# Kernel tuning notes

Hardware: AMD Instinct MI355X
Metric: run time of the kernel (lower is better)

Reference implementation:

```python
import jax, jax.numpy as jnp
import numpy as np

D_MODEL = 1024
EXPAND = 4
D_INNER = EXPAND * D_MODEL  # 4096
D_STATE = 16
D_CONV = 4
DT_RANK = (D_MODEL + 15) // 16  # 64
B_SZ, L_SEQ = 2, 2048
EPS = 1e-5


def _quantize(w):
    # round(clamp(w / mean|w|, -1, 1)) -> ternary weights
    s = w / (jnp.mean(jnp.abs(w)) + 1e-8)
    return jnp.round(jnp.clip(s, -1.0, 1.0))


def setup_inputs() -> dict:
    key = jax.random.key(0)
    ks = jax.random.split(key, 16)
    f32 = jnp.float32
    x = jax.random.normal(ks[0], (B_SZ, L_SEQ, D_MODEL), dtype=f32)
    # LayerNorms
    g1 = jnp.ones((D_MODEL,), f32); b1 = jnp.zeros((D_MODEL,), f32)
    g2 = jnp.ones((D_MODEL,), f32); b2 = jnp.zeros((D_MODEL,), f32)
    # SwiGLU MLP (ternary-quantized weights, as in __init__)
    w1 = _quantize(jax.random.normal(ks[1], (EXPAND * D_MODEL, D_MODEL), f32) * 0.02)
    bias1 = jnp.zeros((EXPAND * D_MODEL,), f32)
    w2 = _quantize(jax.random.normal(ks[2], (D_MODEL, EXPAND * D_MODEL), f32) * 0.02)
    bias2 = jnp.zeros((D_MODEL,), f32)
    # Mamba params
    in_proj_w = jax.random.normal(ks[3], (2 * D_INNER, D_MODEL), f32) * 0.02
    conv_w = jax.random.normal(ks[4], (D_INNER, D_CONV), f32) * 0.2
    conv_b = jnp.zeros((D_INNER,), f32)
    x_proj_w = jax.random.normal(ks[5], (DT_RANK + 2 * D_STATE, D_INNER), f32) * 0.02
    dt_proj_w = jax.random.normal(ks[6], (D_INNER, DT_RANK), f32) * (DT_RANK ** -0.5)
    dt_proj_b = jnp.log(jnp.expm1(jnp.clip(
        jnp.exp(jax.random.uniform(ks[7], (D_INNER,), f32) * (np.log(0.1) - np.log(1e-3)) + np.log(1e-3)),
        1e-4, None)))  # standard mamba dt bias init
    A_log = jnp.log(jnp.broadcast_to(jnp.arange(1, D_STATE + 1, dtype=f32), (D_INNER, D_STATE)))
    D = jnp.ones((D_INNER,), f32)
    out_proj_w = jax.random.normal(ks[8], (D_MODEL, D_INNER), f32) * 0.02
    return dict(x=x, g1=g1, b1=b1, g2=g2, b2=b2, w1=w1, bias1=bias1, w2=w2, bias2=bias2,
                in_proj_w=in_proj_w, conv_w=conv_w, conv_b=conv_b, x_proj_w=x_proj_w,
                dt_proj_w=dt_proj_w, dt_proj_b=dt_proj_b, A_log=A_log, D=D,
                out_proj_w=out_proj_w)


def _layernorm(x, g, b):
    mu = jnp.mean(x, -1, keepdims=True)
    var = jnp.mean(jnp.square(x - mu), -1, keepdims=True)
    return (x - mu) * jax.lax.rsqrt(var + EPS) * g + b


def _mamba(xn, in_proj_w, conv_w, conv_b, x_proj_w, dt_proj_w, dt_proj_b, A_log, D, out_proj_w):
    B, L, _ = xn.shape
    xz = jnp.einsum('bld,ed->ble', xn, in_proj_w)  # [B,L,2*d_inner]
    u, z = jnp.split(xz, 2, axis=-1)
    # causal depthwise conv1d, kernel size D_CONV
    up = jnp.pad(u, ((0, 0), (D_CONV - 1, 0), (0, 0)))
    conv = conv_b + sum(up[:, k:k + L, :] * conv_w[:, k] for k in range(D_CONV))
    u = jax.nn.silu(conv)  # [B,L,d_inner]
    x_dbl = jnp.einsum('bld,ed->ble', u, x_proj_w)
    dt_in, Bm, Cm = jnp.split(x_dbl, [DT_RANK, DT_RANK + D_STATE], axis=-1)
    dt = jax.nn.softplus(jnp.einsum('blr,dr->bld', dt_in, dt_proj_w) + dt_proj_b)
    A = -jnp.exp(A_log)  # [d_inner, d_state]

    def step(h, inp):
        dt_t, B_t, C_t, u_t = inp  # [B,d_inner],[B,d_state],[B,d_state],[B,d_inner]
        dA = jnp.exp(dt_t[..., None] * A)              # [B,d_inner,d_state]
        h = dA * h + (dt_t * u_t)[..., None] * B_t[:, None, :]
        y = jnp.einsum('bds,bs->bd', h, C_t)
        return h, y

    h0 = jnp.zeros((B, D_INNER, D_STATE), xn.dtype)
    xs = (dt.swapaxes(0, 1), Bm.swapaxes(0, 1), Cm.swapaxes(0, 1), u.swapaxes(0, 1))
    _, ys = jax.lax.scan(step, h0, xs)
    y = ys.swapaxes(0, 1) + u * D
    y = y * jax.nn.silu(z)
    return jnp.einsum('ble,de->bld', y, out_proj_w)


def reference(x, g1, b1, g2, b2, w1, bias1, w2, bias2, in_proj_w, conv_w, conv_b,
              x_proj_w, dt_proj_w, dt_proj_b, A_log, D, out_proj_w):
    h = _layernorm(x, g1, b1)
    h = jax.nn.silu(jnp.einsum('bld,ed->ble', h, w1) + bias1)
    x = x + jnp.einsum('ble,de->bld', h, w2) + bias2
    x = x + _mamba(_layernorm(x, g2, b2), in_proj_w, conv_w, conv_b, x_proj_w,
                   dt_proj_w, dt_proj_b, A_log, D, out_proj_w)
    return x
```

## Files before the change

kernel.cpp:

```cpp
#include <hip/hip_runtime.h>
#include <cstdint>
#include <cstddef>


namespace {
constexpr int D_MODEL = 1024;
constexpr int D_INNER = 4096;
constexpr int D_STATE = 16;
constexpr int DT_RANK = 64;
constexpr int B_SZ    = 2;
constexpr int L_SEQ   = 2048;
constexpr int M_ROWS  = B_SZ * L_SEQ;
constexpr int LC      = 64;
constexpr int NCHUNK  = L_SEQ / LC;
}

typedef __bf16 bf16x8_t __attribute__((ext_vector_type(8)));
typedef float  f32x4    __attribute__((ext_vector_type(4)));

__device__ __forceinline__ unsigned short f2bf(float f) {
  union { float f; unsigned int u; } v; v.f = f;
  unsigned int r = (v.u + 0x7fffu + ((v.u >> 16) & 1u)) >> 16;
  return (unsigned short)r;
}
__device__ __forceinline__ float bf2f(unsigned short s) {
  union { unsigned int u; float f; } v; v.u = ((unsigned int)s) << 16;
  return v.f;
}

__device__ __forceinline__ float softplus_fast(float v) {
  const float e = __builtin_amdgcn_exp2f(-fabsf(v) * 1.44269504088896f);
  return fmaxf(v, 0.f) + 0.693147180559945f * __builtin_amdgcn_logf(1.f + e);
}

__device__ __forceinline__ void gload16(const void* g, void* l) {
  __builtin_amdgcn_global_load_lds(
      (const __attribute__((address_space(1))) unsigned int*)g,
      (__attribute__((address_space(3))) unsigned int*)l, 16, 0, 0);
}

__global__ __launch_bounds__(256)
void cvt6(const float* __restrict__ s0, unsigned short* __restrict__ d0,
          const float* __restrict__ s1, unsigned short* __restrict__ d1,
          const float* __restrict__ s2, unsigned short* __restrict__ d2,
          const float* __restrict__ s3, unsigned short* __restrict__ d3,
          const float* __restrict__ s4, unsigned short* __restrict__ d4,
          const float* __restrict__ s5, unsigned short* __restrict__ d5) {
  int blk = blockIdx.x;
  const float* s; unsigned short* d;
  if (blk < 4096)                  { s = s0; d = d0; }
  else if ((blk -= 4096) < 4096)   { s = s1; d = d1; }
  else if ((blk -= 4096) < 8192)   { s = s2; d = d2; }
  else if ((blk -= 8192) < 384)    { s = s3; d = d3; }
  else if ((blk -= 384) < 256)     { s = s4; d = d4; }
  else { blk -= 256;                 s = s5; d = d5; }
  const int i = blk * 1024 + threadIdx.x * 4;
  float4 v = *(const float4*)(s + i);
  ushort4 o; o.x = f2bf(v.x); o.y = f2bf(v.y); o.z = f2bf(v.z); o.w = f2bf(v.w);
  *(ushort4*)(d + i) = o;
}

__global__ __launch_bounds__(256) void ln_bf16(const float* __restrict__ x,
                                               const float* __restrict__ g,
                                               const float* __restrict__ b,
                                               unsigned short* __restrict__ out) {
  const int row = blockIdx.x;
  const int tid = threadIdx.x;
  const float4 v = *(const float4*)(x + (size_t)row * D_MODEL + tid * 4);
  float s  = v.x + v.y + v.z + v.w;
  float s2 = v.x*v.x + v.y*v.y + v.z*v.z + v.w*v.w;
#pragma unroll
  for (int o = 32; o >= 1; o >>= 1) { s += __shfl_xor(s, o); s2 += __shfl_xor(s2, o); }
  __shared__ float red[8];
  if ((tid & 63) == 0) { red[(tid >> 6) * 2] = s; red[(tid >> 6) * 2 + 1] = s2; }
  __syncthreads();
  s  = red[0] + red[2] + red[4] + red[6];
  s2 = red[1] + red[3] + red[5] + red[7];
  const float mu  = s * (1.f / D_MODEL);
  const float var = s2 * (1.f / D_MODEL) - mu * mu;
  const float rstd = rsqrtf(var + 1e-5f);
  const float4 gv = *(const float4*)(g + tid * 4);
  const float4 bv = *(const float4*)(b + tid * 4);
  ushort4 o;
  o.x = f2bf((v.x - mu) * rstd * gv.x + bv.x);
  o.y = f2bf((v.y - mu) * rstd * gv.y + bv.y);
  o.z = f2bf((v.z - mu) * rstd * gv.z + bv.z);
  o.w = f2bf((v.w - mu) * rstd * gv.w + bv.w);
  *(ushort4*)(out + (size_t)row * D_MODEL + tid * 4) = o;
}

__global__ __launch_bounds__(256)
void combine_ln(const float* __restrict__ part, const float* __restrict__ bias,
                const float* __restrict__ res, const float* __restrict__ g,
                const float* __restrict__ b, float* __restrict__ x2out,
                unsigned short* __restrict__ xnout) {
  const int row = blockIdx.x;
  const int tid = threadIdx.x;
  const size_t i4 = (size_t)row * D_MODEL + tid * 4;
  constexpr size_t S = (size_t)M_ROWS * D_MODEL;
  const float4 p0 = *(const float4*)(part + i4);
  const float4 p1 = *(const float4*)(part + S + i4);
  const float4 p2 = *(const float4*)(part + 2 * S + i4);
  const float4 p3 = *(const float4*)(part + 3 * S + i4);
  const float4 bv = *(const float4*)(bias + tid * 4);
  const float4 rv = *(const float4*)(res + i4);
  float4 v;
  v.x = p0.x + p1.x + p2.x + p3.x + bv.x + rv.x;
  v.y = p0.y + p1.y + p2.y + p3.y + bv.y + rv.y;
  v.z = p0.z + p1.z + p2.z + p3.z + bv.z + rv.z;
  v.w = p0.w + p1.w + p2.w + p3.w + bv.w + rv.w;
  *(float4*)(x2out + i4) = v;
  float s  = v.x + v.y + v.z + v.w;
  float s2 = v.x*v.x + v.y*v.y + v.z*v.z + v.w*v.w;
#pragma unroll
  for (int o = 32; o >= 1; o >>= 1) { s += __shfl_xor(s, o); s2 += __shfl_xor(s2, o); }
  __shared__ float red[8];
  if ((tid & 63) == 0) { red[(tid >> 6) * 2] = s; red[(tid >> 6) * 2 + 1] = s2; }
  __syncthreads();
  s  = red[0] + red[2] + red[4] + red[6];
  s2 = red[1] + red[3] + red[5] + red[7];
  const float mu  = s * (1.f / D_MODEL);
  const float var = s2 * (1.f / D_MODEL) - mu * mu;
  const float rstd = rsqrtf(var + 1e-5f);
  const float4 gv = *(const float4*)(g + tid * 4);
  const float4 b2 = *(const float4*)(b + tid * 4);
  ushort4 o;
  o.x = f2bf((v.x - mu) * rstd * gv.x + b2.x);
  o.y = f2bf((v.y - mu) * rstd * gv.y + b2.y);
  o.z = f2bf((v.z - mu) * rstd * gv.z + b2.z);
  o.w = f2bf((v.w - mu) * rstd * gv.w + b2.w);
  *(ushort4*)(xnout + i4) = o;
}

template<int EPI>
__global__ __launch_bounds__(512, 1)
void gemm256(const unsigned short* __restrict__ A, const unsigned short* __restrict__ W,
             int M, int N, int K, int lda, int ldw,
             const float* __restrict__ bias, void* __restrict__ out0) {
  __shared__ unsigned short As[2][256 * 64];
  __shared__ unsigned short Bs[2][256 * 64];
  const int tid  = threadIdx.x;
  const int w    = tid >> 6;
  const int lane = tid & 63;
  const int wr = w >> 2;
  const int wc = w & 3;
  const int fr = lane & 15;
  const int fq = lane >> 4;

  const int gx = gridDim.x, gy = gridDim.y;
  const int nwg = gx * gy;
  const int id  = blockIdx.y * gx + blockIdx.x;
  const int wid = (id & 7) * (nwg >> 3) + (id >> 3);
  const int n0 = (wid / gy) * 256;
  const int m0 = (wid % gy) * 256;

  const int srow  = tid >> 3;
  const int skelem = ((tid & 7) ^ (srow & 7)) * 8;

  int aslot[2];
#pragma unroll
  for (int ks = 0; ks < 2; ++ks) aslot[ks] = ((ks * 4 + fq) ^ (fr & 7)) * 8;

  f32x4 acc[8][4];
#pragma unroll
  for (int m = 0; m < 8; ++m)
#pragma unroll
    for (int n = 0; n < 4; ++n) acc[m][n] = f32x4{0.f, 0.f, 0.f, 0.f};

  const int NT = K >> 6;

  auto STAGE_HALF = [&](int half, int tn, unsigned short* Ad, unsigned short* Bd) {
    const int k0 = tn * 64;
    if (half < 2) {
#pragma unroll
      for (int li = 0; li < 2; ++li) {
        const int l = half * 2 + li;
        gload16(A + (size_t)(m0 + l * 64 + srow) * lda + k0 + skelem,
                Ad + (l * 64 + w * 8) * 64);
      }
    } else {
#pragma unroll
      for (int li = 0; li < 2; ++li) {
        const int l = (half - 2) * 2 + li;
        gload16(W + (size_t)(n0 + l * 64 + srow) * ldw + k0 + skelem,
                Bd + (l * 64 + w * 8) * 64);
      }
    }
  };

#pragma unroll
  for (int h = 0; h < 4; ++h) STAGE_HALF(h, 0, &As[0][0], &Bs[0][0]);
  asm volatile("s_waitcnt vmcnt(0)" ::: "memory");
  __builtin_amdgcn_sched_barrier(0);
  __builtin_amdgcn_s_barrier();
  __builtin_amdgcn_sched_barrier(0);

  for (int t = 0; t < NT; ++t) {
    const int cur = t & 1;
    const unsigned short* Ab = &As[cur][0];
    const unsigned short* Bb = &Bs[cur][0];
    unsigned short* Adn = &As[cur ^ 1][0];
    unsigned short* Bdn = &Bs[cur ^ 1][0];
    const bool more = (t + 1 < NT);
#pragma unroll
    for (int p = 0; p < 4; ++p) {
      const int qm = p & 1, qn = p >> 1;
      bf16x8_t af[4][2], bf[2][2];
#pragma unroll
      for (int mfi = 0; mfi < 4; ++mfi)
#pragma unroll
        for (int ks = 0; ks < 2; ++ks)
          af[mfi][ks] = *(const bf16x8_t*)
              &Ab[(wr * 128 + (qm * 4 + mfi) * 16 + fr) * 64 + aslot[ks]];
#pragma unroll
      for (int nfi = 0; nfi < 2; ++nfi)
#pragma unroll
        for (int ks = 0; ks < 2; ++ks)
          bf[nfi][ks] = *(const bf16x8_t*)
              &Bb[(wc * 64 + (qn * 2 + nfi) * 16 + fr) * 64 + aslot[ks]];
      if (more) STAGE_HALF(p, t + 1, Adn, Bdn);
      asm volatile("s_waitcnt lgkmcnt(0)" ::: "memory");
      __builtin_amdgcn_sched_barrier(0);
      __builtin_amdgcn_s_barrier();
      __builtin_amdgcn_sched_barrier(0);
      __builtin_amdgcn_s_setprio(1);
#pragma unroll
      for (int mfi = 0; mfi < 4; ++mfi)
#pragma unroll
        for (int nfi = 0; nfi < 2; ++nfi)
#pragma unroll
          for (int ks = 0; ks < 2; ++ks)
            acc[qm * 4 + mfi][qn * 2 + nfi] = __builtin_amdgcn_mfma_f32_16x16x32_bf16(
                af[mfi][ks], bf[nfi][ks], acc[qm * 4 + mfi][qn * 2 + nfi], 0, 0, 0);
      __builtin_amdgcn_s_setprio(0);
      __builtin_amdgcn_sched_barrier(0);
    }
    asm volatile("s_waitcnt vmcnt(0)" ::: "memory");
    __builtin_amdgcn_sched_barrier(0);
    __builtin_amdgcn_s_barrier();
    __builtin_amdgcn_sched_barrier(0);
  }

#pragma unroll
  for (int mf = 0; mf < 8; ++mf)
#pragma unroll
    for (int nf = 0; nf < 4; ++nf)
#pragma unroll
      for (int j = 0; j < 4; ++j) {
        const int r = m0 + wr * 128 + mf * 16 + fq * 4 + j;
        const int c = n0 + wc * 64 + nf * 16 + fr;
        float v = acc[mf][nf][j];
        if constexpr (EPI == 0) {
          v += bias[c];
          v = v / (1.f + __expf(-v));
          ((unsigned short*)out0)[(size_t)r * N + c] = f2bf(v);
        } else {
          ((unsigned short*)out0)[(size_t)r * N + c] = f2bf(v);
        }
      }
}

template<int EPI>
__global__ __launch_bounds__(256)
void gemm_bt(const unsigned short* __restrict__ A, const unsigned short* __restrict__ W,
             int M, int N, int K, int lda, int ldw, int ldc,
             const float* __restrict__ bias, const float* __restrict__ res,
             void* __restrict__ out0) {
  if constexpr (EPI == 6 || EPI == 8) {
    const size_t koff = (size_t)blockIdx.z * K;
    A += koff; W += koff;
    if constexpr (EPI == 6)
      out0 = (void*)((float*)out0 + (size_t)blockIdx.z * M * ldc);
    else
      out0 = (void*)((unsigned short*)out0 + (size_t)blockIdx.z * M * ldc);
  }
  const int gx = gridDim.x, gy = gridDim.y;
  const int nwg = gx * gy;
  const int id  = blockIdx.y * gx + blockIdx.x;
  const int wid = (id & 7) * (nwg >> 3) + (id >> 3);
  const int n0 = (wid / gy) * 128;
  const int m0 = (wid % gy) * 128;

  __shared__ unsigned short As[2][128 * 32];
  __shared__ unsigned short Bs[2][128 * 32];
  const int tid  = threadIdx.x;
  const int w    = tid >> 6;
  const int lane = tid & 63;
  const int wm = (w >> 1) * 64;
  const int wn = (w & 1) * 64;
  const int lrow = lane >> 2;
  const int lkb  = (lane & 3) * 8;
  const int fr   = lane & 15;
  const int fq   = lane >> 4;

  f32x4 acc[4][4];
#pragma unroll
  for (int m = 0; m < 4; ++m)
#pragma unroll
    for (int n = 0; n < 4; ++n) acc[m][n] = f32x4{0.f, 0.f, 0.f, 0.f};

  const int ar0 = m0 + (w * 2 + 0) * 16 + lrow;
  const int ar1 = m0 + (w * 2 + 1) * 16 + lrow;
  int br0 = n0 + (w * 2 + 0) * 16 + lrow; if (br0 > N - 1) br0 = N - 1;
  int br1 = n0 + (w * 2 + 1) * 16 + lrow; if (br1 > N - 1) br1 = N - 1;

  const int nk = K >> 5;
  auto STAGE = [&](int buf, int kt) {
    const int k0 = kt * 32;
    gload16(A + (size_t)ar0 * lda + k0 + lkb, &As[buf][(w * 2 + 0) * 512]);
    gload16(A + (size_t)ar1 * lda + k0 + lkb, &As[buf][(w * 2 + 1) * 512]);
    gload16(W + (size_t)br0 * ldw + k0 + lkb, &Bs[buf][(w * 2 + 0) * 512]);
    gload16(W + (size_t)br1 * ldw + k0 + lkb, &Bs[buf][(w * 2 + 1) * 512]);
  };
  STAGE(0, 0);
  if (nk > 1) STAGE(1, 1);

  for (int kt = 0; kt < nk; ++kt) {
    const int cur = kt & 1;
    if (kt + 1 < nk) asm volatile("s_waitcnt vmcnt(4)" ::: "memory");
    else             asm volatile("s_waitcnt vmcnt(0)" ::: "memory");
    __builtin_amdgcn_sched_barrier(0);
    __builtin_amdgcn_s_barrier();
    __builtin_amdgcn_sched_barrier(0);
    bf16x8_t af[4], bf[4];
#pragma unroll
    for (int m = 0; m < 4; ++m) af[m] = *(const bf16x8_t*)&As[cur][(wm + m * 16 + fr) * 32 + fq * 8];
#pragma unroll
    for (int n = 0; n < 4; ++n) bf[n] = *(const bf16x8_t*)&Bs[cur][(wn + n * 16 + fr) * 32 + fq * 8];
    __builtin_amdgcn_s_setprio(1);
#pragma unroll
    for (int m = 0; m < 4; ++m)
#pragma unroll
      for (int n = 0; n < 4; ++n)
        acc[m][n] = __builtin_amdgcn_mfma_f32_16x16x32_bf16(af[m], bf[n], acc[m][n], 0, 0, 0);
    __builtin_amdgcn_s_setprio(0);
    __builtin_amdgcn_sched_barrier(0);
    asm volatile("s_waitcnt lgkmcnt(0)" ::: "memory");
    __builtin_amdgcn_s_barrier();
    __builtin_amdgcn_sched_barrier(0);
    if (kt + 2 < nk) STAGE(cur, kt + 2);
  }

#pragma unroll
  for (int m = 0; m < 4; ++m)
#pragma unroll
    for (int n = 0; n < 4; ++n)
#pragma unroll
      for (int j = 0; j < 4; ++j) {
        const int r = m0 + wm + m * 16 + fq * 4 + j;
        const int c = n0 + wn + n * 16 + fr;
        if (c >= N) continue;
        float v = acc[m][n][j];
        if constexpr (EPI == 4) {
          v = softplus_fast(v + bias[c]);
          ((unsigned short*)out0)[(size_t)r * ldc + c] = f2bf(v);
        } else if constexpr (EPI == 6) {
          ((float*)out0)[(size_t)r * ldc + c] = v;
        } else {
          ((unsigned short*)out0)[(size_t)r * ldc + c] = f2bf(v);
        }
      }
}

__global__ __launch_bounds__(256)
void splitk_combine_bf(const unsigned short* __restrict__ part,
                       const float* __restrict__ res, float* __restrict__ out) {
  const size_t i4 = ((size_t)blockIdx.x * 256 + threadIdx.x) * 4;
  constexpr size_t S = (size_t)M_ROWS * D_MODEL;
  float a0 = 0.f, a1 = 0.f, a2 = 0.f, a3 = 0.f;
#pragma unroll
  for (int z = 0; z < 4; ++z) {
    const ushort4 p = *(const ushort4*)(part + z * S + i4);
    a0 += bf2f(p.x); a1 += bf2f(p.y); a2 += bf2f(p.z); a3 += bf2f(p.w);
  }
  const float4 r = *(const float4*)(res + i4);
  *(float4*)(out + i4) = float4{a0 + r.x, a1 + r.y, a2 + r.z, a3 + r.w};
}

__global__ __launch_bounds__(256)
void conv_silu_k(const unsigned short* __restrict__ xz, const float* __restrict__ cw,
                 const float* __restrict__ cb, unsigned short* __restrict__ uc) {
  const size_t idx = (size_t)blockIdx.x * 256 + threadIdx.x;
  const int d   = (int)(idx & (D_INNER - 1));
  const int row = (int)(idx >> 12);
  const int l   = row & (L_SEQ - 1);
  const float4 w4 = *(const float4*)(cw + d * 4);
  const unsigned short* up = xz + (size_t)row * (2 * D_INNER) + d;
  float acc = cb[d];
  if (l >= 3) acc += bf2f(up[-(ptrdiff_t)3 * 2 * D_INNER]) * w4.x;
  if (l >= 2) acc += bf2f(up[-(ptrdiff_t)2 * 2 * D_INNER]) * w4.y;
  if (l >= 1) acc += bf2f(up[-(ptrdiff_t)1 * 2 * D_INNER]) * w4.z;
  acc += bf2f(up[0]) * w4.w;
  const float r = acc / (1.f + __expf(-acc));
  uc[(size_t)row * D_INNER + d] = f2bf(r);
}

__global__ __launch_bounds__(256)
void xproj_combine(const float* __restrict__ part, unsigned short* __restrict__ dtin,
                   float* __restrict__ Bm, float* __restrict__ Cm) {
  const int idx = blockIdx.x * 256 + threadIdx.x;
  const int r = idx / 96, c = idx - r * 96;
  constexpr size_t S = (size_t)M_ROWS * 96;
  const float v = part[idx] + part[idx + S] + part[idx + 2 * S] + part[idx + 3 * S];
  if (c < DT_RANK)            dtin[(size_t)r * DT_RANK + c] = f2bf(v);
  else if (c < DT_RANK + 16)  Bm[(size_t)r * 16 + (c - DT_RANK)] = v;
  else                        Cm[(size_t)r * 16 + (c - DT_RANK - 16)] = v;
}

__global__ __launch_bounds__(128)
void scan_part(const unsigned short* __restrict__ dt, const unsigned short* __restrict__ uc,
               const float* __restrict__ Bm, const float* __restrict__ A_log,
               float* __restrict__ Q, float* __restrict__ sumdt) {
  __shared__ float sB[LC][D_STATE];
  const int lt = threadIdx.x;
  const int d  = blockIdx.x * 128 + lt;
  const int c  = blockIdx.y;
  const int b  = blockIdx.z;
  const size_t rowbase = (size_t)b * L_SEQ + (size_t)c * LC;
#pragma unroll
  for (int i = 0; i < 2; ++i)
    ((float4*)&sB[0][0])[lt + i * 128] =
        ((const float4*)(Bm + rowbase * D_STATE))[lt + i * 128];
  float Ap[D_STATE];
#pragma unroll
  for (int s = 0; s < D_STATE; ++s)
    Ap[s] = -__expf(A_log[d * D_STATE + s]) * 1.44269504088896f;
  float h[D_STATE];
#pragma unroll
  for (int s = 0; s < D_STATE; ++s) h[s] = 0.f;
  float sdt = 0.f;
  __syncthreads();
  for (int t = 0; t < LC; ++t) {
    const size_t row = rowbase + t;
    const float dtv = bf2f(dt[row * D_INNER + d]);
    const float uv  = bf2f(uc[row * D_INNER + d]);
    sdt += dtv;
    const float du = dtv * uv;
    const float4* bp = (const float4*)&sB[t][0];
    const float4 b0 = bp[0], b1 = bp[1], b2 = bp[2], b3 = bp[3];
    const float Bv[16] = {b0.x,b0.y,b0.z,b0.w, b1.x,b1.y,b1.z,b1.w,
                          b2.x,b2.y,b2.z,b2.w, b3.x,b3.y,b3.z,b3.w};
#pragma unroll
    for (int s = 0; s < D_STATE; ++s) {
      const float dA = __builtin_amdgcn_exp2f(dtv * Ap[s]);
      h[s] = fmaf(dA, h[s], du * Bv[s]);
    }
  }
  float* q = Q + ((((size_t)b * NCHUNK + c) * D_INNER + d) << 4);
#pragma unroll
  for (int s = 0; s < D_STATE; s += 4)
    *(float4*)(q + s) = float4{h[s], h[s+1], h[s+2], h[s+3]};
  sumdt[((size_t)b * NCHUNK + c) * D_INNER + d] = sdt;
}

__global__ __launch_bounds__(256)
void scan_carry(float* __restrict__ Q, const float* __restrict__ sumdt,
                const float* __restrict__ A_log) {
  const int idx = blockIdx.x * 256 + threadIdx.x;
  const int s = idx & 15;
  const int d = (idx >> 4) & (D_INNER - 1);
  const int b = idx >> 16;
  const float Ap = -__expf(A_log[d * D_STATE + s]) * 1.44269504088896f;
  float h = 0.f;
  for (int c = 0; c < NCHUNK; ++c) {
    const size_t base = ((size_t)b * NCHUNK + c) * D_INNER;
    const size_t qoff = ((base + d) << 4) + s;
    const float q = Q[qoff];
    const float P = __builtin_amdgcn_exp2f(sumdt[base + d] * Ap);
    Q[qoff] = h;
    h = fmaf(P, h, q);
  }
}

__global__ __launch_bounds__(128)
void scan_final(const unsigned short* __restrict__ dt, const unsigned short* __restrict__ uc,
                const float* __restrict__ Bm, const float* __restrict__ Cm,
                unsigned short* __restrict__ xz, const float* __restrict__ A_log,
                const float* __restrict__ Dvec, const float* __restrict__ Hin) {
  __shared__ float sB[LC][D_STATE];
  __shared__ float sC[LC][D_STATE];
  const int lt = threadIdx.x;
  const int d  = blockIdx.x * 128 + lt;
  const int c  = blockIdx.y;
  const int b  = blockIdx.z;
  const size_t rowbase = (size_t)b * L_SEQ + (size_t)c * LC;
#pragma unroll
  for (int i = 0; i < 2; ++i) {
    ((float4*)&sB[0][0])[lt + i * 128] =
        ((const float4*)(Bm + rowbase * D_STATE))[lt + i * 128];
    ((float4*)&sC[0][0])[lt + i * 128] =
        ((const float4*)(Cm + rowbase * D_STATE))[lt + i * 128];
  }
  float Ap[D_STATE];
#pragma unroll
  for (int s = 0; s < D_STATE; ++s)
    Ap[s] = -__expf(A_log[d * D_STATE + s]) * 1.44269504088896f;
  float h[D_STATE];
  const float* hin = Hin + ((((size_t)b * NCHUNK + c) * D_INNER + d) << 4);
#pragma unroll
  for (int s = 0; s < D_STATE; s += 4) {
    const float4 hv = *(const float4*)(hin + s);
    h[s] = hv.x; h[s+1] = hv.y; h[s+2] = hv.z; h[s+3] = hv.w;
  }
  const float Dv = Dvec[d];
  __syncthreads();
  for (int t = 0; t < LC; ++t) {
    const size_t row = rowbase + t;
    const float dtv = bf2f(dt[row * D_INNER + d]);
    const float uv  = bf2f(uc[row * D_INNER + d]);
    const float zv  = bf2f(xz[row * (2 * D_INNER) + D_INNER + d]);
    const float du = dtv * uv;
    const float4* bp = (const float4*)&sB[t][0];
    const float4 b0 = bp[0], b1 = bp[1], b2 = bp[2], b3 = bp[3];
    const float Bv[16] = {b0.x,b0.y,b0.z,b0.w, b1.x,b1.y,b1.z,b1.w,
                          b2.x,b2.y,b2.z,b2.w, b3.x,b3.y,b3.z,b3.w};
    const float4* cp = (const float4*)&sC[t][0];
    const float4 c0 = cp[0], c1 = cp[1], c2 = cp[2], c3 = cp[3];
    const float Cv[16] = {c0.x,c0.y,c0.z,c0.w, c1.x,c1.y,c1.z,c1.w,
                          c2.x,c2.y,c2.z,c2.w, c3.x,c3.y,c3.z,c3.w};
    float y0 = 0.f, y1 = 0.f;
#pragma unroll
    for (int s = 0; s < D_STATE; s += 2) {
      const float dA0 = __builtin_amdgcn_exp2f(dtv * Ap[s]);
      const float dA1 = __builtin_amdgcn_exp2f(dtv * Ap[s+1]);
      h[s]   = fmaf(dA0, h[s],   du * Bv[s]);
      h[s+1] = fmaf(dA1, h[s+1], du * Bv[s+1]);
      y0 = fmaf(h[s],   Cv[s],   y0);
      y1 = fmaf(h[s+1], Cv[s+1], y1);
    }
    const float yo = (y0 + y1 + uv * Dv) * (zv / (1.f + __expf(-zv)));
    xz[row * (2 * D_INNER) + d] = f2bf(yo);
  }
}

extern "C" void kernel_launch(void* const* d_in, const int* in_sizes, int n_in,
                              void* d_out, int out_size, void* d_ws, size_t ws_size,
                              hipStream_t stream) {
  (void)in_sizes; (void)n_in; (void)out_size; (void)ws_size;
  const float* x     = (const float*)d_in[0];
  const float* g1    = (const float*)d_in[1];
  const float* b1    = (const float*)d_in[2];
  const float* g2    = (const float*)d_in[3];
  const float* b2    = (const float*)d_in[4];
  const float* w1    = (const float*)d_in[5];
  const float* bias1 = (const float*)d_in[6];
  const float* w2    = (const float*)d_in[7];
  const float* bias2 = (const float*)d_in[8];
  const float* ipw   = (const float*)d_in[9];
  const float* cw    = (const float*)d_in[10];
  const float* cb    = (const float*)d_in[11];
  const float* xpw   = (const float*)d_in[12];
  const float* dtw   = (const float*)d_in[13];
  const float* dtbv  = (const float*)d_in[14];
  const float* A_log = (const float*)d_in[15];
  const float* Dvec  = (const float*)d_in[16];
  const float* opw   = (const float*)d_in[17];

  char* ws = (char*)d_ws;
  size_t off = 0;
  auto alloc = [&](size_t bytes) { void* p = ws + off; off = (off + bytes + 255) & ~(size_t)255; return p; };

  unsigned short* w1b  = (unsigned short*)alloc((size_t)D_INNER * D_MODEL * 2);
  unsigned short* w2b  = (unsigned short*)alloc((size_t)D_MODEL * D_INNER * 2);
  unsigned short* ipb  = (unsigned short*)alloc((size_t)2 * D_INNER * D_MODEL * 2);
  unsigned short* xpb  = (unsigned short*)alloc((size_t)96 * D_INNER * 2);
  unsigned short* dtb  = (unsigned short*)alloc((size_t)D_INNER * DT_RANK * 2);
  unsigned short* opb  = (unsigned short*)alloc((size_t)D_MODEL * D_INNER * 2);
  unsigned short* xn   = (unsigned short*)alloc((size_t)M_ROWS * D_MODEL * 2);
  unsigned short* hid  = (unsigned short*)alloc((size_t)M_ROWS * D_INNER * 2);
  float*          x2   = (float*)alloc((size_t)M_ROWS * D_MODEL * 4);
  unsigned short* xz   = (unsigned short*)alloc((size_t)M_ROWS * 2 * D_INNER * 2);
  unsigned short* dtbf = (unsigned short*)alloc((size_t)M_ROWS * D_INNER * 2);
  unsigned short* dtin = (unsigned short*)alloc((size_t)M_ROWS * DT_RANK * 2);
  float*          Bmb  = (float*)alloc((size_t)M_ROWS * 16 * 4);
  float*          Cmb  = (float*)alloc((size_t)M_ROWS * 16 * 4);
  float*          xpart= (float*)alloc((size_t)4 * M_ROWS * 96 * 4);
  float*          Qbuf = (float*)alloc((size_t)B_SZ * NCHUNK * D_INNER * 16 * 4);
  unsigned short* ucb  = hid;
  float*          sumdt = xpart;
  float*          pA   = (float*)xz;
  unsigned short* pB   = dtbf;

  cvt6<<<21120, 256, 0, stream>>>(w1, w1b, w2, w2b, ipw, ipb, xpw, xpb, dtw, dtb, opw, opb);

  ln_bf16<<<M_ROWS, 256, 0, stream>>>(x, g1, b1, xn);
  gemm256<0><<<dim3(D_INNER / 256, M_ROWS / 256), 512, 0, stream>>>(
      xn, w1b, M_ROWS, D_INNER, D_MODEL, D_MODEL, D_MODEL, bias1, hid);
  gemm_bt<6><<<dim3(D_MODEL / 128, M_ROWS / 128, 4), 256, 0, stream>>>(
      hid, w2b, M_ROWS, D_MODEL, D_INNER / 4, D_INNER, D_INNER, D_MODEL, nullptr, nullptr, pA);
  combine_ln<<<M_ROWS, 256, 0, stream>>>(pA, bias2, x, g2, b2, x2, xn);

  gemm256<2><<<dim3(2 * D_INNER / 256, M_ROWS / 256), 512, 0, stream>>>(
      xn, ipb, M_ROWS, 2 * D_INNER, D_MODEL, D_MODEL, D_MODEL, nullptr, xz);
  conv_silu_k<<<(size_t)M_ROWS * D_INNER / 256, 256, 0, stream>>>(xz, cw, cb, ucb);

  gemm_bt<6><<<dim3(1, M_ROWS / 128, 4), 256, 0, stream>>>(
      ucb, xpb, M_ROWS, 96, 1024, D_INNER, D_INNER, 96,
      nullptr, nullptr, xpart);
  xproj_combine<<<M_ROWS * 96 / 256, 256, 0, stream>>>(xpart, dtin, Bmb, Cmb);

  gemm_bt<4><<<dim3(D_INNER / 128, M_ROWS / 128), 256, 0, stream>>>(
      dtin, dtb, M_ROWS, D_INNER, DT_RANK, DT_RANK, DT_RANK, D_INNER, dtbv, nullptr, dtbf);

  scan_part<<<dim3(D_INNER / 128, NCHUNK, B_SZ), 128, 0, stream>>>(
      dtbf, ucb, Bmb, A_log, Qbuf, sumdt);
  scan_carry<<<B_SZ * D_INNER * 16 / 256, 256, 0, stream>>>(Qbuf, sumdt, A_log);
  scan_final<<<dim3(D_INNER / 128, NCHUNK, B_SZ), 128, 0, stream>>>(
      dtbf, ucb, Bmb, Cmb, xz, A_log, Dvec, Qbuf);

  gemm_bt<8><<<dim3(D_MODEL / 128, M_ROWS / 128, 4), 256, 0, stream>>>(
      xz, opb, M_ROWS, D_MODEL, D_INNER / 4, 2 * D_INNER, D_INNER, D_MODEL,
      nullptr, nullptr, pB);
  splitk_combine_bf<<<M_ROWS * D_MODEL / 1024, 256, 0, stream>>>(pB, x2, (float*)d_out);
}
```

Before: 526.6 us.

## Restructure GEMM main loop into 4-buffer K=32 pipeline with three-deep prefetch

Replaces the double-buffered K=64 tiles, which are consumed in four sub-phases, with a four-slot ring of K=32 sub-tiles. Loads run three stages ahead, using vmcnt-based partial waits. The aim is to hide global-load latency better and drop the per-quarter barriers, leaving one compute block and two barriers per 32-wide K step. In exchange there are more loop iterations and barriers per unit of K. The new LDS swizzle on 32-element rows may also raise bank conflicts.

```diff
diff --git a/kernel.cpp b/kernel.cpp
--- a/kernel.cpp
+++ b/kernel.cpp
@@ -137,8 +137,8 @@
 void gemm256(const unsigned short* __restrict__ A, const unsigned short* __restrict__ W,
              int M, int N, int K, int lda, int ldw,
              const float* __restrict__ bias, void* __restrict__ out0) {
-  __shared__ unsigned short As[2][256 * 64];
-  __shared__ unsigned short Bs[2][256 * 64];
+  __shared__ unsigned short As[4][256 * 32];
+  __shared__ unsigned short Bs[4][256 * 32];
   const int tid  = threadIdx.x;
   const int w    = tid >> 6;
   const int lane = tid & 63;
@@ -154,12 +154,9 @@
   const int n0 = (wid / gy) * 256;
   const int m0 = (wid % gy) * 256;
 
-  const int srow  = tid >> 3;
-  const int skelem = ((tid & 7) ^ (srow & 7)) * 8;
-
-  int aslot[2];
-#pragma unroll
-  for (int ks = 0; ks < 2; ++ks) aslot[ks] = ((ks * 4 + fq) ^ (fr & 7)) * 8;
+  const int srow   = tid >> 2;
+  const int skelem = ((tid & 3) ^ (srow & 3)) * 8;
+  const int aslot  = (fq ^ (fr & 3)) * 8;
 
   f32x4 acc[8][4];
 #pragma unroll
@@ -167,75 +164,51 @@
 #pragma unroll
     for (int n = 0; n < 4; ++n) acc[m][n] = f32x4{0.f, 0.f, 0.f, 0.f};
 
-  const int NT = K >> 6;
-
-  auto STAGE_HALF = [&](int half, int tn, unsigned short* Ad, unsigned short* Bd) {
-    const int k0 = tn * 64;
-    if (half < 2) {
-#pragma unroll
-      for (int li = 0; li < 2; ++li) {
-        const int l = half * 2 + li;
-        gload16(A + (size_t)(m0 + l * 64 + srow) * lda + k0 + skelem,
-                Ad + (l * 64 + w * 8) * 64);
-      }
-    } else {
-#pragma unroll
-      for (int li = 0; li < 2; ++li) {
-        const int l = (half - 2) * 2 + li;
-        gload16(W + (size_t)(n0 + l * 64 + srow) * ldw + k0 + skelem,
-                Bd + (l * 64 + w * 8) * 64);
-      }
+  const int NS = K >> 5;
+
+  auto STAGE_SUB = [&](int s) {
+    const int k0 = s << 5;
+    const int b  = s & 3;
+#pragma unroll
+    for (int half = 0; half < 2; ++half) {
+      gload16(A + (size_t)(m0 + half * 128 + srow) * lda + k0 + skelem,
+              &As[b][(half * 128 + w * 16) * 32]);
+      gload16(W + (size_t)(n0 + half * 128 + srow) * ldw + k0 + skelem,
+              &Bs[b][(half * 128 + w * 16) * 32]);
     }
   };
 
-#pragma unroll
-  for (int h = 0; h < 4; ++h) STAGE_HALF(h, 0, &As[0][0], &Bs[0][0]);
-  asm volatile("s_waitcnt vmcnt(0)" ::: "memory");
+  STAGE_SUB(0); STAGE_SUB(1); STAGE_SUB(2);
+  asm volatile("s_waitcnt vmcnt(8)" ::: "memory");
   __builtin_amdgcn_sched_barrier(0);
   __builtin_amdgcn_s_barrier();
   __builtin_amdgcn_sched_barrier(0);
 
-  for (int t = 0; t < NT; ++t) {
-    const int cur = t & 1;
-    const unsigned short* Ab = &As[cur][0];
-    const unsigned short* Bb = &Bs[cur][0];
-    unsigned short* Adn = &As[cur ^ 1][0];
-    unsigned short* Bdn = &Bs[cur ^ 1][0];
-    const bool more = (t + 1 < NT);
-#pragma unroll
-    for (int p = 0; p < 4; ++p) {
-      const int qm = p & 1, qn = p >> 1;
-      bf16x8_t af[4][2], bf[2][2];
-#pragma unroll
-      for (int mfi = 0; mfi < 4; ++mfi)
-#pragma unroll
-        for (int ks = 0; ks < 2; ++ks)
-          af[mfi][ks] = *(const bf16x8_t*)
-              &Ab[(wr * 128 + (qm * 4 + mfi) * 16 + fr) * 64 + aslot[ks]];
-#pragma unroll
-      for (int nfi = 0; nfi < 2; ++nfi)
-#pragma unroll
-        for (int ks = 0; ks < 2; ++ks)
-          bf[nfi][ks] = *(const bf16x8_t*)
-              &Bb[(wc * 64 + (qn * 2 + nfi) * 16 + fr) * 64 + aslot[ks]];
-      if (more) STAGE_HALF(p, t + 1, Adn, Bdn);
-      asm volatile("s_waitcnt lgkmcnt(0)" ::: "memory");
-      __builtin_amdgcn_sched_barrier(0);
-      __builtin_amdgcn_s_barrier();
-      __builtin_amdgcn_sched_barrier(0);
-      __builtin_amdgcn_s_setprio(1);
-#pragma unroll
-      for (int mfi = 0; mfi < 4; ++mfi)
-#pragma unroll
-        for (int nfi = 0; nfi < 2; ++nfi)
-#pragma unroll
-          for (int ks = 0; ks < 2; ++ks)
-            acc[qm * 4 + mfi][qn * 2 + nfi] = __builtin_amdgcn_mfma_f32_16x16x32_bf16(
-                af[mfi][ks], bf[nfi][ks], acc[qm * 4 + mfi][qn * 2 + nfi], 0, 0, 0);
-      __builtin_amdgcn_s_setprio(0);
-      __builtin_amdgcn_sched_barrier(0);
-    }
-    asm volatile("s_waitcnt vmcnt(0)" ::: "memory");
+  for (int s = 0; s < NS; ++s) {
+    const unsigned short* Ab = &As[s & 3][0];
+    const unsigned short* Bb = &Bs[s & 3][0];
+    bf16x8_t af[8], bf[4];
+#pragma unroll
+    for (int m = 0; m < 8; ++m)
+      af[m] = *(const bf16x8_t*)&Ab[(wr * 128 + m * 16 + fr) * 32 + aslot];
+#pragma unroll
+    for (int n = 0; n < 4; ++n)
+      bf[n] = *(const bf16x8_t*)&Bb[(wc * 64 + n * 16 + fr) * 32 + aslot];
+    if (s + 3 < NS) STAGE_SUB(s + 3);
+    __builtin_amdgcn_s_barrier();
+    asm volatile("s_waitcnt lgkmcnt(0)" ::: "memory");
+    __builtin_amdgcn_sched_barrier(0);
+    __builtin_amdgcn_s_setprio(1);
+#pragma unroll
+    for (int m = 0; m < 8; ++m)
+#pragma unroll
+      for (int n = 0; n < 4; ++n)
+        acc[m][n] = __builtin_amdgcn_mfma_f32_16x16x32_bf16(af[m], bf[n], acc[m][n], 0, 0, 0);
+    __builtin_amdgcn_s_setprio(0);
+    __builtin_amdgcn_sched_barrier(0);
+    if (s + 3 < NS)      asm volatile("s_waitcnt vmcnt(8)" ::: "memory");
+    else if (s + 2 < NS) asm volatile("s_waitcnt vmcnt(4)" ::: "memory");
+    else if (s + 1 < NS) asm volatile("s_waitcnt vmcnt(0)" ::: "memory");
     __builtin_amdgcn_sched_barrier(0);
     __builtin_amdgcn_s_barrier();
     __builtin_amdgcn_sched_barrier(0);
```

Result: no change. 531.5 us (+0.9%).
